# Performance work log

Hardware: AMD Instinct MI355X
Metric: run time of the kernel (lower is better)

The kernel has to match this reference:

```python
import jax, jax.numpy as jnp
import numpy as np

K = 3
KK = K * K


def _conv1x1(x, w, b):
    # x: [B,Ci,H,W], w: [Co,Ci]
    return jnp.einsum('bihw,oi->bohw', x, w) + b[None, :, None, None]


def _conv3x3(x, w, b):
    y = jax.lax.conv_general_dilated(x, w, (1, 1), ((1, 1), (1, 1)),
                                     dimension_numbers=('NCHW', 'OIHW', 'NCHW'))
    return y + b[None, :, None, None]


def _deform_conv3x3(x, offset, w, b):
    # Deformable conv v1, kernel 3x3, stride 1, pad 1, dilation 1, 1 deformable group.
    # x: [B,C,H,W]; offset: [B,2*KK,H,W] (dy,dx interleaved per kernel tap); w: [Co,C,3,3]
    B, C, H, W = x.shape
    dt = x.dtype
    off = offset.reshape(B, KK, 2, H, W)
    ky, kx = jnp.meshgrid(jnp.arange(K, dtype=dt), jnp.arange(K, dtype=dt), indexing='ij')
    ky = ky.reshape(KK)
    kx = kx.reshape(KK)
    # sampling locations: out_pos - pad + kernel_tap + learned offset
    base_y = jnp.arange(H, dtype=dt) - 1.0  # pad = 1
    base_x = jnp.arange(W, dtype=dt) - 1.0
    sy = base_y[None, None, :, None] + ky[None, :, None, None] + off[:, :, 0]  # [B,KK,H,W]
    sx = base_x[None, None, None, :] + kx[None, :, None, None] + off[:, :, 1]
    y0 = jnp.floor(sy)
    x0 = jnp.floor(sx)
    ty = sy - y0
    tx = sx - x0

    def gather(iy, ix):
        valid = ((iy >= 0) & (iy <= H - 1) & (ix >= 0) & (ix <= W - 1)).astype(dt)
        iyc = jnp.clip(iy, 0, H - 1).astype(jnp.int32)
        ixc = jnp.clip(ix, 0, W - 1).astype(jnp.int32)
        vals = jax.vmap(lambda img, a, c: img[:, a, c])(x, iyc, ixc)  # [B,C,KK,H,W]
        return vals * valid[:, None]

    w00 = ((1 - ty) * (1 - tx))[:, None]
    w01 = ((1 - ty) * tx)[:, None]
    w10 = (ty * (1 - tx))[:, None]
    w11 = (ty * tx)[:, None]
    sampled = (gather(y0, x0) * w00 + gather(y0, x0 + 1) * w01 +
               gather(y0 + 1, x0) * w10 + gather(y0 + 1, x0 + 1) * w11)  # [B,C,KK,H,W]
    Co = w.shape[0]
    out = jnp.einsum('bikhw,oik->bohw', sampled, w.reshape(Co, C, KK))
    return out + b[None, :, None, None]


def _branch(features, dw, db, ow, ob, tw, tb):
    h = _conv1x1(features, dw, db)
    off = _conv3x3(h, ow, ob)  # offset-predicting conv inside DFConv2d
    return jax.nn.relu(_deform_conv3x3(h, off, tw, tb))


def setup_inputs() -> dict:
    key = jax.random.key(0)
    ks = jax.random.split(key, 13)
    C = 256
    s1 = 1.0 / np.sqrt(C)          # kaiming_normal a=1 for 1x1 conv
    s3 = 1.0 / np.sqrt(C * KK)     # 3x3 conv
    so = 0.01                       # small offset-conv weights -> modest offsets
    f = lambda k, s, sc: jax.random.normal(k, s, dtype=jnp.float32) * sc
    return {
        'features': f(ks[0], (4, C, 64, 64), 1.0),
        'agg_down_w': f(ks[1], (C, C), s1),
        'agg_down_b': jnp.zeros((C,), jnp.float32),
        'agg_off_w': f(ks[2], (2 * KK, C, K, K), so),
        'agg_off_b': jnp.zeros((2 * KK,), jnp.float32),
        'agg_w': f(ks[3], (C, C, K, K), s3),
        'agg_b': jnp.zeros((C,), jnp.float32),
        'appr_down_w': f(ks[4], (C, C), s1),
        'appr_down_b': jnp.zeros((C,), jnp.float32),
        'appr_off_w': f(ks[5], (2 * KK, C, K, K), so),
        'appr_off_b': jnp.zeros((2 * KK,), jnp.float32),
        'appr_w': f(ks[6], (C, C, K, K), s3),
        'appr_b': jnp.zeros((C,), jnp.float32),
    }


def reference(features, agg_down_w, agg_down_b, agg_off_w, agg_off_b, agg_w, agg_b,
              appr_down_w, appr_down_b, appr_off_w, appr_off_b, appr_w, appr_b):
    agg = _branch(features, agg_down_w, agg_down_b, agg_off_w, agg_off_b, agg_w, agg_b)
    appr = _branch(features, appr_down_w, appr_down_b, appr_off_w, appr_off_b, appr_w, appr_b)
    return (agg, appr)
```

## Files before the change

### kernel.cpp

```cpp
#include <hip/hip_runtime.h>

#define HWP 4096
#define NPIX 4194304
#define KDIM 2304

typedef __attribute__((ext_vector_type(4))) float f32x4;
typedef __attribute__((ext_vector_type(4))) int   i32x4;
typedef __attribute__((ext_vector_type(8))) short short8;
typedef __attribute__((ext_vector_type(4))) unsigned short bf16x4;

__device__ __forceinline__ unsigned short bf16_rne(float f) {
    unsigned int u = __builtin_bit_cast(unsigned int, f);
    u += 0x7FFFu + ((u >> 16) & 1u);
    return (unsigned short)(u >> 16);
}

__device__ __forceinline__ float bf2f(unsigned short u) {
    return __builtin_bit_cast(float, (unsigned int)u << 16);
}

__device__ __forceinline__ unsigned int cvt_pk_bf16(float lo, float hi) {
    unsigned int r;
    asm("v_cvt_pk_bf16_f32 %0, %1, %2" : "=v"(r) : "v"(lo), "v"(hi));
    return r;
}

__device__ __forceinline__ void gload_lds16(const void* g, void* l) {
    __builtin_amdgcn_global_load_lds((const __attribute__((address_space(1))) void*)g,
                                     (__attribute__((address_space(3))) void*)l, 16, 0, 0);
}

__global__ void prep_all_kernel(const float* __restrict__ x, unsigned short* __restrict__ fbt,
                                const float* __restrict__ dw0, const float* __restrict__ dw1,
                                const float* __restrict__ tw0, const float* __restrict__ tw1,
                                const float* __restrict__ ow0, const float* __restrict__ ow1,
                                unsigned short* __restrict__ w1b2,
                                unsigned short* __restrict__ w2A,
                                unsigned short* __restrict__ w2o) {
    __shared__ float T[64][65];
    int b = blockIdx.x;
    int t = threadIdx.x;
    if (b < 1024) {
        int pt = b & 63, ct = (b >> 6) & 3, bb = b >> 8;
        int lane = t & 63;
        int r = t >> 6;
        int c0 = ct * 64, p0 = pt * 64;
        const float* xb = x + (size_t)(bb * 256 + c0) * HWP + p0;
#pragma unroll
        for (int rr = 0; rr < 16; ++rr) {
            int ci = r * 16 + rr;
            T[ci][lane] = xb[(size_t)ci * HWP + lane];
        }
        __syncthreads();
        unsigned short* ob = fbt + ((size_t)bb * HWP + p0) * 256 + c0;
#pragma unroll
        for (int rr = 0; rr < 16; ++rr) {
            int px = r * 16 + rr;
            ob[(size_t)px * 256 + lane] = bf16_rne(T[lane][px]);
        }
        return;
    }
    int idx = (b - 1024) * 256 + t;
    if (idx < 131072) {
        int br = idx >> 16;
        int i  = idx & 65535;
        const float* dw = br ? dw1 : dw0;
        w1b2[idx] = bf16_rne(dw[i]);
    } else if (idx < 131072 + 1179648) {
        int j = idx - 131072;
        int br = j >= 589824;
        int i  = br ? j - 589824 : j;
        const float* tw = br ? tw1 : tw0;
        int ci = i & 255;
        int r  = i >> 8;
        int tap = r % 9;
        int o   = r / 9;
        w2A[j] = bf16_rne(tw[(o * 256 + ci) * 9 + tap]);
    } else {
        int j = idx - 131072 - 1179648;
        int br = j >= 73728;
        int i  = br ? j - 73728 : j;
        const float* ow = br ? ow1 : ow0;
        int m = i / 2304;
        int k = i - m * 2304;
        int tap = k >> 8;
        int ci  = k & 255;
        w2o[j] = (m < 18) ? bf16_rne(ow[(m * 256 + ci) * 9 + tap]) : (unsigned short)0;
    }
}

__global__ void prep_w2_kernel(const float* __restrict__ tw0, const float* __restrict__ tw1,
                               unsigned short* __restrict__ w2) {
    int idx = blockIdx.x * 256 + threadIdx.x;
    int br = idx >= 589824;
    int i  = br ? idx - 589824 : idx;
    const float* tw = br ? tw1 : tw0;
    int ci = i & 255;
    int r  = i >> 8;
    int tap = r % 9;
    int o   = r / 9;
    w2[idx] = bf16_rne(tw[(o * 256 + ci) * 9 + tap]);
}

__global__ void prep_ow2_kernel(const float* __restrict__ ow0, const float* __restrict__ ow1,
                                float* __restrict__ owt) {
    int idx = blockIdx.x * 256 + threadIdx.x;
    int br = idx >= 41472;
    int i  = br ? idx - 41472 : idx;
    const float* ow = br ? ow1 : ow0;
    int co = i % 18;
    int r  = i / 18;
    int k  = r % 9;
    int ci = r / 9;
    owt[idx] = ow[(co * 256 + ci) * 9 + k];
}

__global__ void prep_w12_kernel(const float* __restrict__ dw0, const float* __restrict__ dw1,
                                unsigned short* __restrict__ w1b) {
    int idx = blockIdx.x * 256 + threadIdx.x;
    int br = idx >> 16;
    int i  = idx & 65535;
    const float* dw = br ? dw1 : dw0;
    w1b[idx] = bf16_rne(dw[i]);
}

__global__ void prep_fb16_kernel(const float* __restrict__ x, unsigned short* __restrict__ fbt) {
    __shared__ float T[64][65];
    int pt = blockIdx.x;
    int ct = blockIdx.y;
    int bb = blockIdx.z;
    int t = threadIdx.x;
    int lane = t & 63;
    int r = t >> 6;
    int c0 = ct * 64, p0 = pt * 64;
    const float* xb = x + (size_t)(bb * 256 + c0) * HWP + p0;
#pragma unroll
    for (int rr = 0; rr < 16; ++rr) {
        int ci = r * 16 + rr;
        T[ci][lane] = xb[(size_t)ci * HWP + lane];
    }
    __syncthreads();
    unsigned short* ob = fbt + ((size_t)bb * HWP + p0) * 256 + c0;
#pragma unroll
    for (int rr = 0; rr < 16; ++rr) {
        int px = r * 16 + rr;
        ob[(size_t)px * 256 + lane] = bf16_rne(T[lane][px]);
    }
}

__launch_bounds__(256)
__global__ void gemm1x1_kernel(const unsigned short* __restrict__ w1b2,
                               const unsigned short* __restrict__ fbt,
                               const float* __restrict__ db0, const float* __restrict__ db1,
                               float* __restrict__ h2, unsigned short* __restrict__ ht2,
                               int write_h) {
    __shared__ unsigned short As[128 * 64];
    __shared__ unsigned short Bs[64 * 64];
    int pt = blockIdx.x;
    int ot = blockIdx.y;
    int z  = blockIdx.z;
    int bb = z & 3;
    int br = z >> 2;
    const unsigned short* w1b = w1b2 + (size_t)br * 65536;
    const float* db = br ? db1 : db0;
    int t  = threadIdx.x;
    int l  = t & 63;
    int w  = t >> 6;
    int wr = w >> 1, wc = w & 1;
    int o0 = ot * 128, p0 = pt * 64;
    const unsigned short* fb = fbt + (size_t)bb * HWP * 256;
    f32x4 acc[4][2];
#pragma unroll
    for (int i = 0; i < 4; ++i)
#pragma unroll
        for (int j = 0; j < 2; ++j) acc[i][j] = (f32x4){0.f, 0.f, 0.f, 0.f};

    for (int ks = 0; ks < 4; ++ks) {
        int k0 = ks * 64;
#pragma unroll
        for (int rA = 0; rA < 4; ++rA) {
            int s = rA * 256 + t;
            int row = s >> 3, cg = (s & 7) ^ (row & 7);
            gload_lds16(w1b + (size_t)(o0 + row) * 256 + k0 + cg * 8, As + s * 8);
        }
#pragma unroll
        for (int rB = 0; rB < 2; ++rB) {
            int s = rB * 256 + t;
            int row = s >> 3, cg = (s & 7) ^ (row & 7);
            gload_lds16(fb + (size_t)(p0 + row) * 256 + k0 + cg * 8, Bs + s * 8);
        }
        __syncthreads();
#pragma unroll
        for (int half = 0; half < 2; ++half) {
            short8 a[4], b[2];
#pragma unroll
            for (int fr = 0; fr < 4; ++fr) {
                int row = wr * 64 + fr * 16 + (l & 15);
                int oct = half * 4 + (l >> 4);
                a[fr] = *reinterpret_cast<const short8*>(As + row * 64 + ((oct ^ (row & 7)) * 8));
            }
#pragma unroll
            for (int fc = 0; fc < 2; ++fc) {
                int row = wc * 32 + fc * 16 + (l & 15);
                int oct = half * 4 + (l >> 4);
                b[fc] = *reinterpret_cast<const short8*>(Bs + row * 64 + ((oct ^ (row & 7)) * 8));
            }
#pragma unroll
            for (int fr = 0; fr < 4; ++fr)
#pragma unroll
                for (int fc = 0; fc < 2; ++fc)
                    acc[fr][fc] = __builtin_amdgcn_mfma_f32_16x16x32_bf16(a[fr], b[fc], acc[fr][fc], 0, 0, 0);
        }
        __syncthreads();
    }

    float* hb = h2 + (size_t)br * NPIX + (size_t)bb * 256 * HWP;
    unsigned short* htb = ht2 + (size_t)br * NPIX + (size_t)bb * HWP * 256;
#pragma unroll
    for (int fr = 0; fr < 4; ++fr) {
        int o = o0 + wr * 64 + fr * 16 + ((l >> 4) << 2);
#pragma unroll
        for (int fc = 0; fc < 2; ++fc) {
            int p = p0 + wc * 32 + fc * 16 + (l & 15);
            f32x4 v;
#pragma unroll
            for (int reg = 0; reg < 4; ++reg) {
                v[reg] = acc[fr][fc][reg] + db[o + reg];
                if (write_h) hb[(size_t)(o + reg) * HWP + p] = v[reg];
            }
            uint2 pk;
            pk.x = cvt_pk_bf16(v[0], v[1]);
            pk.y = cvt_pk_bf16(v[2], v[3]);
            *reinterpret_cast<uint2*>(htb + (size_t)p * 256 + o) = pk;
        }
    }
}

__launch_bounds__(256)
__global__ void off_mfma_kernel(const unsigned short* __restrict__ w2o,
                                const unsigned short* __restrict__ ht2,
                                const float* __restrict__ ob0, const float* __restrict__ ob1,
                                float* __restrict__ off2) {
    __shared__ float red[4][1152];
    int id = blockIdx.x;
    int br = id >> 8;
    int bb = (id >> 6) & 3;
    int y  = id & 63;
    const unsigned short* wA = w2o + (size_t)br * 73728;
    const unsigned short* htb = ht2 + (size_t)br * NPIX + (size_t)bb * HWP * 256;
    const float* ob = br ? ob1 : ob0;
    int t = threadIdx.x;
    int l = t & 63;
    int w = t >> 6;
    short8 zero = {};
    f32x4 acc[2][4];
#pragma unroll
    for (int i = 0; i < 2; ++i)
#pragma unroll
        for (int j = 0; j < 4; ++j) acc[i][j] = (f32x4){0.f, 0.f, 0.f, 0.f};

    for (int tap = 0; tap < 9; ++tap) {
        int ky = tap / 3, kx = tap % 3;
        int yy = y + ky - 1;
        bool vy = (yy >= 0) && (yy < 64);
        int cyy = min(max(yy, 0), 63);
#pragma unroll
        for (int sh = 0; sh < 2; ++sh) {
            int s = w * 2 + sh;
            short8 a[2], b[4];
#pragma unroll
            for (int fr = 0; fr < 2; ++fr)
                a[fr] = *reinterpret_cast<const short8*>(
                    wA + (size_t)(fr * 16 + (l & 15)) * KDIM + tap * 256 + s * 32 + ((l >> 4) << 3));
#pragma unroll
            for (int fc = 0; fc < 4; ++fc) {
                int px = fc * 16 + (l & 15);
                int xx = px + kx - 1;
                bool v = vy && (xx >= 0) && (xx < 64);
                int cxx = min(max(xx, 0), 63);
                short8 bv = *reinterpret_cast<const short8*>(
                    htb + (size_t)(cyy * 64 + cxx) * 256 + s * 32 + ((l >> 4) << 3));
                b[fc] = v ? bv : zero;
            }
#pragma unroll
            for (int fr = 0; fr < 2; ++fr)
#pragma unroll
                for (int fc = 0; fc < 4; ++fc)
                    acc[fr][fc] = __builtin_amdgcn_mfma_f32_16x16x32_bf16(a[fr], b[fc], acc[fr][fc], 0, 0, 0);
        }
    }

#pragma unroll
    for (int fr = 0; fr < 2; ++fr)
#pragma unroll
        for (int fc = 0; fc < 4; ++fc) {
            int px = fc * 16 + (l & 15);
#pragma unroll
            for (int reg = 0; reg < 4; ++reg) {
                int co = fr * 16 + ((l >> 4) << 2) + reg;
                if (co < 18) red[w][co * 64 + px] = acc[fr][fc][reg];
            }
        }
    __syncthreads();
    float* offb = off2 + (size_t)br * 294912 + (size_t)(bb * 18) * HWP + y * 64;
    for (int e = t; e < 1152; e += 256) {
        int co = e >> 6, px = e & 63;
        float ssum = ob[co] + red[0][e] + red[1][e] + red[2][e] + red[3][e];
        offb[(size_t)co * HWP + px] = ssum;
    }
}

__global__ void off_conv_part_kernel(const float* __restrict__ h2, const float* __restrict__ owt2,
                                     float* __restrict__ part2) {
    int y  = blockIdx.x & 63;
    int bb = blockIdx.x >> 6;
    int c  = blockIdx.y;
    int br = blockIdx.z;
    const float* h = h2 + (size_t)br * NPIX;
    const float* owt = owt2 + (size_t)br * 41472;
    float* part = part2 + (size_t)br * 2359296;
    int t  = threadIdx.x;
    int x  = t & 63;
    int wv = __builtin_amdgcn_readfirstlane(t >> 6);
    int  toff[9];
    bool tval[9];
#pragma unroll
    for (int ky = 0; ky < 3; ++ky) {
        int yy = y + ky - 1;
        bool vy = (yy >= 0) && (yy < 64);
        int cyy = min(max(yy, 0), 63);
#pragma unroll
        for (int kx = 0; kx < 3; ++kx) {
            int xx = x + kx - 1;
            tval[ky * 3 + kx] = vy && (xx >= 0) && (xx < 64);
            toff[ky * 3 + kx] = cyy * 64 + min(max(xx, 0), 63);
        }
    }
    float acc[18];
#pragma unroll
    for (int co = 0; co < 18; ++co) acc[co] = 0.f;
    int ci0 = c * 32 + wv * 8;
    const float* hb = h + (size_t)(bb * 256 + ci0) * HWP;
#pragma unroll
    for (int i = 0; i < 8; ++i) {
        const float* hc = hb + i * HWP;
        const float* wci = owt + (size_t)(ci0 + i) * 162;
#pragma unroll
        for (int k = 0; k < 9; ++k) {
            float hv = hc[toff[k]];
            hv = tval[k] ? hv : 0.f;
            const float* wk = wci + k * 18;
#pragma unroll
            for (int co = 0; co < 18; ++co)
                acc[co] = fmaf(wk[co], hv, acc[co]);
        }
    }
    __shared__ float red[4][18][64];
    int wvl = t >> 6;
#pragma unroll
    for (int co = 0; co < 18; ++co) red[wvl][co][x] = acc[co];
    __syncthreads();
    if (wvl == 0) {
#pragma unroll
        for (int co = 0; co < 18; ++co) {
            float s = red[0][co][x] + red[1][co][x] + red[2][co][x] + red[3][co][x];
            part[(size_t)c * 294912 + ((bb * 18 + co) << 12) + (y << 6) + x] = s;
        }
    }
}

__global__ void off_reduce2_kernel(const float* __restrict__ part2,
                                   const float* __restrict__ ob0, const float* __restrict__ ob1,
                                   float* __restrict__ off2) {
    int idx = blockIdx.x * 256 + threadIdx.x;
    int br = idx >= 294912;
    int i  = br ? idx - 294912 : idx;
    const float* part = part2 + (size_t)br * 2359296;
    const float* b = br ? ob1 : ob0;
    int co = (i >> 12) % 18;
    float s = b[co];
#pragma unroll
    for (int c = 0; c < 8; ++c) s += part[(size_t)c * 294912 + i];
    off2[idx] = s;
}

__launch_bounds__(512, 4)
__global__ void dgemm_fused_kernel(const unsigned short* __restrict__ w2b,
                                   const unsigned short* __restrict__ ht2,
                                   const float* __restrict__ off2,
                                   const float* __restrict__ tb0,
                                   const float* __restrict__ tb1,
                                   float* __restrict__ out) {
    __shared__ unsigned short As[2][8][1024];
    __shared__ unsigned short Bs[64 * 256];
    int id = blockIdx.x;
    int sw = (id & 7) * 64 + (id >> 3);
    int br = sw >> 8;
    int mt = sw & 255;
    int bb = mt >> 6;
    int y  = mt & 63;
    const unsigned short* w2 = w2b + (size_t)br * 589824;
    const unsigned short* htb = ht2 + (size_t)br * NPIX + (size_t)bb * HWP * 256;
    const float* offb = off2 + (size_t)br * 294912 + (size_t)(bb * 18) * HWP + y * 64;
    const float* bias = br ? tb1 : tb0;
    int t = threadIdx.x;
    int l = t & 63;
    int w = t >> 6;
    int wvu = __builtin_amdgcn_readfirstlane(w);

    f32x4 acc[2][4];
#pragma unroll
    for (int i = 0; i < 2; ++i)
#pragma unroll
        for (int j = 0; j < 4; ++j) acc[i][j] = (f32x4){0.f, 0.f, 0.f, 0.f};

#define STAGE_AS(buf, ss)                                                          \
    do {                                                                           \
        _Pragma("unroll")                                                          \
        for (int r_ = 0; r_ < 2; ++r_) {                                           \
            int idx_ = r_ * 64 + l;                                                \
            int row_ = idx_ >> 2;                                                  \
            int kc_ = (idx_ & 3) ^ ((row_ >> 1) & 3);                              \
            gload_lds16(wtap + (size_t)(wvu * 32 + row_) * KDIM + (ss) * 32 + kc_ * 8, \
                        &As[buf][wvu][idx_ * 8]);                                  \
        }                                                                          \
    } while (0)

    for (int tap = 0; tap < 9; ++tap) {
        int ky = tap / 3, kx = tap % 3;
        const unsigned short* wtap = w2 + tap * 256;
        __syncthreads();
        STAGE_AS(0, 0);
#pragma unroll
        for (int i = 0; i < 8; ++i) {
            int px = wvu * 8 + i;
            float dy = offb[(size_t)(2 * tap) * HWP + px];
            float dx = offb[(size_t)(2 * tap + 1) * HWP + px];
            float sy = (float)(y - 1 + ky) + dy;
            float sx = (float)(px - 1 + kx) + dx;
            float y0f = floorf(sy), x0f = floorf(sx);
            float ty = sy - y0f, tx = sx - x0f;
            int iy0 = (int)y0f, ix0 = (int)x0f;
            int iy1 = iy0 + 1, ix1 = ix0 + 1;
            bool vy0 = (iy0 >= 0) & (iy0 < 64);
            bool vy1 = (iy1 >= 0) & (iy1 < 64);
            bool vx0 = (ix0 >= 0) & (ix0 < 64);
            bool vx1 = (ix1 >= 0) & (ix1 < 64);
            int cy0 = min(max(iy0, 0), 63), cy1 = min(max(iy1, 0), 63);
            int cx0 = min(max(ix0, 0), 63), cx1 = min(max(ix1, 0), 63);
            float w00 = (1.f - ty) * (1.f - tx) * ((vy0 & vx0) ? 1.f : 0.f);
            float w01 = (1.f - ty) * tx * ((vy0 & vx1) ? 1.f : 0.f);
            float w10 = ty * (1.f - tx) * ((vy1 & vx0) ? 1.f : 0.f);
            float w11 = ty * tx * ((vy1 & vx1) ? 1.f : 0.f);
            int le = l << 2;
            bf16x4 q00 = *reinterpret_cast<const bf16x4*>(htb + ((cy0 * 64 + cx0) << 8) + le);
            bf16x4 q01 = *reinterpret_cast<const bf16x4*>(htb + ((cy0 * 64 + cx1) << 8) + le);
            bf16x4 q10 = *reinterpret_cast<const bf16x4*>(htb + ((cy1 * 64 + cx0) << 8) + le);
            bf16x4 q11 = *reinterpret_cast<const bf16x4*>(htb + ((cy1 * 64 + cx1) << 8) + le);
            f32x4 s;
#pragma unroll
            for (int j = 0; j < 4; ++j)
                s[j] = fmaf(w00, bf2f(q00[j]),
                       fmaf(w01, bf2f(q01[j]),
                       fmaf(w10, bf2f(q10[j]), w11 * bf2f(q11[j]))));
            uint2 pk;
            pk.x = cvt_pk_bf16(s[0], s[1]);
            pk.y = cvt_pk_bf16(s[2], s[3]);
            int g = l >> 1, sub = l & 1;
            *reinterpret_cast<uint2*>(Bs + px * 256 + (((g ^ (px & 7)) << 3) | (sub << 2))) = pk;
        }
        __syncthreads();
        for (int s = 0; s < 8; ++s) {
            if (s < 7) {
                int buf = (s + 1) & 1;
                STAGE_AS(buf, s + 1);
            }
            asm volatile("s_waitcnt vmcnt(2)" ::: "memory");
            __builtin_amdgcn_sched_barrier(0);
            short8 a[2], b[4];
#pragma unroll
            for (int fr = 0; fr < 2; ++fr) {
                int rowl = fr * 16 + (l & 15);
                int oct = (l >> 4) ^ ((rowl >> 1) & 3);
                a[fr] = *reinterpret_cast<const short8*>(&As[s & 1][wvu][rowl * 32 + oct * 8]);
            }
#pragma unroll
            for (int fc = 0; fc < 4; ++fc) {
                int prow = fc * 16 + (l & 15);
                int cg8 = (s << 2) + (l >> 4);
                b[fc] = *reinterpret_cast<const short8*>(Bs + prow * 256 + ((cg8 ^ (prow & 7)) << 3));
            }
            __builtin_amdgcn_s_setprio(1);
#pragma unroll
            for (int fr = 0; fr < 2; ++fr)
#pragma unroll
                for (int fc = 0; fc < 4; ++fc)
                    acc[fr][fc] = __builtin_amdgcn_mfma_f32_16x16x32_bf16(a[fr], b[fc], acc[fr][fc], 0, 0, 0);
            __builtin_amdgcn_s_setprio(0);
        }
    }
#undef STAGE_AS

    float* outp = out + (size_t)br * NPIX + (size_t)(bb * 256) * HWP + y * 64;
#pragma unroll
    for (int fr = 0; fr < 2; ++fr) {
        int o = w * 32 + fr * 16 + ((l >> 4) << 2);
#pragma unroll
        for (int fc = 0; fc < 4; ++fc) {
            int pxc = fc * 16 + (l & 15);
#pragma unroll
            for (int reg = 0; reg < 4; ++reg) {
                float v = acc[fr][fc][reg] + bias[o + reg];
                outp[(size_t)(o + reg) * HWP + pxc] = fmaxf(v, 0.f);
            }
        }
    }
}

__launch_bounds__(256)
__global__ void sample2_kernel(const unsigned short* __restrict__ ht, const float* __restrict__ off,
                               unsigned short* __restrict__ sm, int b0) {
    int y   = blockIdx.x;
    int tap = blockIdx.y;
    int bb  = b0 + blockIdx.z;
    int t   = threadIdx.x;
    int lane = t & 63;
    int wv  = t >> 6;
    int ky = tap / 3, kx = tap % 3;
    const unsigned short* htb = ht + (size_t)bb * HWP * 256;
    const float* offy = off + ((bb * 18 + 2 * tap) * 64 + y) * 64;
    const float* offx = off + ((bb * 18 + 2 * tap + 1) * 64 + y) * 64;
    int mrow = ((bb - b0) * 64 + y) * 64;
#pragma unroll 4
    for (int i = 0; i < 16; ++i) {
        int px = wv * 16 + i;
        float dy = offy[px];
        float dx = offx[px];
        float sy = (float)(y - 1 + ky) + dy;
        float sx = (float)(px - 1 + kx) + dx;
        float y0f = floorf(sy), x0f = floorf(sx);
        float ty = sy - y0f, tx = sx - x0f;
        int iy0 = (int)y0f, ix0 = (int)x0f;
        int iy1 = iy0 + 1, ix1 = ix0 + 1;
        bool vy0 = (iy0 >= 0) & (iy0 < 64);
        bool vy1 = (iy1 >= 0) & (iy1 < 64);
        bool vx0 = (ix0 >= 0) & (ix0 < 64);
        bool vx1 = (ix1 >= 0) & (ix1 < 64);
        int cy0 = min(max(iy0, 0), 63), cy1 = min(max(iy1, 0), 63);
        int cx0 = min(max(ix0, 0), 63), cx1 = min(max(ix1, 0), 63);
        float w00 = (1.f - ty) * (1.f - tx) * ((vy0 & vx0) ? 1.f : 0.f);
        float w01 = (1.f - ty) * tx * ((vy0 & vx1) ? 1.f : 0.f);
        float w10 = ty * (1.f - tx) * ((vy1 & vx0) ? 1.f : 0.f);
        float w11 = ty * tx * ((vy1 & vx1) ? 1.f : 0.f);
        int le = lane << 2;
        bf16x4 q00 = *reinterpret_cast<const bf16x4*>(htb + ((cy0 * 64 + cx0) << 8) + le);
        bf16x4 q01 = *reinterpret_cast<const bf16x4*>(htb + ((cy0 * 64 + cx1) << 8) + le);
        bf16x4 q10 = *reinterpret_cast<const bf16x4*>(htb + ((cy1 * 64 + cx0) << 8) + le);
        bf16x4 q11 = *reinterpret_cast<const bf16x4*>(htb + ((cy1 * 64 + cx1) << 8) + le);
        f32x4 s;
#pragma unroll
        for (int j = 0; j < 4; ++j)
            s[j] = fmaf(w00, bf2f(q00[j]),
                   fmaf(w01, bf2f(q01[j]),
                   fmaf(w10, bf2f(q10[j]), w11 * bf2f(q11[j]))));
        uint2 pk;
        pk.x = cvt_pk_bf16(s[0], s[1]);
        pk.y = cvt_pk_bf16(s[2], s[3]);
        *reinterpret_cast<uint2*>(sm + (size_t)(mrow + px) * KDIM + tap * 256 + lane * 4) = pk;
    }
}

__launch_bounds__(256)
__global__ void gemm2_kernel(const unsigned short* __restrict__ w2b,
                             const unsigned short* __restrict__ smb, size_t smstride,
                             const float* __restrict__ tb0, const float* __restrict__ tb1,
                             float* __restrict__ out, int mbase) {
    __shared__ unsigned short As[128 * 64];
    __shared__ unsigned short Bs[64 * 64];
    int mt = blockIdx.x;
    int ot = blockIdx.y;
    int br = blockIdx.z;
    const unsigned short* w2 = w2b + (size_t)br * 589824;
    const unsigned short* sm = smb + (size_t)br * smstride;
    const float* bias = br ? tb1 : tb0;
    float* outp = out + (size_t)br * NPIX;
    int t  = threadIdx.x;
    int l  = t & 63;
    int w  = t >> 6;
    int wr = w >> 1, wc = w & 1;
    int o0 = ot * 128, m0 = mt * 64;
    f32x4 acc[4][2];
#pragma unroll
    for (int i = 0; i < 4; ++i)
#pragma unroll
        for (int j = 0; j < 2; ++j) acc[i][j] = (f32x4){0.f, 0.f, 0.f, 0.f};

    for (int ks = 0; ks < KDIM / 64; ++ks) {
        int k0 = ks * 64;
#pragma unroll
        for (int rA = 0; rA < 4; ++rA) {
            int s = rA * 256 + t;
            int row = s >> 3, cg = (s & 7) ^ (row & 7);
            gload_lds16(w2 + (size_t)(o0 + row) * KDIM + k0 + cg * 8, As + s * 8);
        }
#pragma unroll
        for (int rB = 0; rB < 2; ++rB) {
            int s = rB * 256 + t;
            int row = s >> 3, cg = (s & 7) ^ (row & 7);
            gload_lds16(sm + (size_t)(m0 + row) * KDIM + k0 + cg * 8, Bs + s * 8);
        }
        __syncthreads();
#pragma unroll
        for (int half = 0; half < 2; ++half) {
            short8 a[4], b[2];
#pragma unroll
            for (int fr = 0; fr < 4; ++fr) {
                int row = wr * 64 + fr * 16 + (l & 15);
                int oct = half * 4 + (l >> 4);
                a[fr] = *reinterpret_cast<const short8*>(As + row * 64 + ((oct ^ (row & 7)) * 8));
            }
#pragma unroll
            for (int fc = 0; fc < 2; ++fc) {
                int row = wc * 32 + fc * 16 + (l & 15);
                int oct = half * 4 + (l >> 4);
                b[fc] = *reinterpret_cast<const short8*>(Bs + row * 64 + ((oct ^ (row & 7)) * 8));
            }
#pragma unroll
            for (int fr = 0; fr < 4; ++fr)
#pragma unroll
                for (int fc = 0; fc < 2; ++fc)
                    acc[fr][fc] = __builtin_amdgcn_mfma_f32_16x16x32_bf16(a[fr], b[fc], acc[fr][fc], 0, 0, 0);
        }
        __syncthreads();
    }

#pragma unroll
    for (int fr = 0; fr < 4; ++fr) {
        int o = o0 + wr * 64 + fr * 16 + ((l >> 4) << 2);
#pragma unroll
        for (int fc = 0; fc < 2; ++fc) {
            int mg = mbase + m0 + wc * 32 + fc * 16 + (l & 15);
            int bbv = mg >> 12;
            int pix = mg & 4095;
            float* op = outp + (size_t)(bbv * 256) * HWP + pix;
#pragma unroll
            for (int reg = 0; reg < 4; ++reg) {
                float v = acc[fr][fc][reg] + bias[o + reg];
                op[(size_t)(o + reg) * HWP] = fmaxf(v, 0.f);
            }
        }
    }
}

extern "C" void kernel_launch(void* const* d_in, const int* in_sizes, int n_in,
                              void* d_out, int out_size, void* d_ws, size_t ws_size,
                              hipStream_t stream) {
    const float* feat = (const float*)d_in[0];
    char* base = (char*)d_ws;
    float* outp = (float*)d_out;
    const size_t perb = (size_t)HWP * KDIM * 2;

    const float* dw0 = (const float*)d_in[1];
    const float* db0 = (const float*)d_in[2];
    const float* ow0 = (const float*)d_in[3];
    const float* ob0 = (const float*)d_in[4];
    const float* tw0 = (const float*)d_in[5];
    const float* tb0 = (const float*)d_in[6];
    const float* dw1 = (const float*)d_in[7];
    const float* db1 = (const float*)d_in[8];
    const float* ow1 = (const float*)d_in[9];
    const float* ob1 = (const float*)d_in[10];
    const float* tw1 = (const float*)d_in[11];
    const float* tb1 = (const float*)d_in[12];

    bool tierA = ws_size >= 47218688;

    if (tierA) {
        unsigned short* ht2 = (unsigned short*)base;
        float* off2 = (float*)(base + 33554432);
        unsigned short* w2A = (unsigned short*)(base + 35913728);
        unsigned short* w2o = (unsigned short*)(base + 38273024);
        unsigned short* fbt = (unsigned short*)(base + 38567936);
        unsigned short* w1b2 = (unsigned short*)(base + 46956544);

        hipLaunchKernelGGL(prep_all_kernel, dim3(6720), dim3(256), 0, stream,
                           feat, fbt, dw0, dw1, tw0, tw1, ow0, ow1, w1b2, w2A, w2o);
        hipLaunchKernelGGL(gemm1x1_kernel, dim3(64, 2, 8), dim3(256), 0, stream,
                           w1b2, fbt, db0, db1, (float*)nullptr, ht2, 0);
        hipLaunchKernelGGL(off_mfma_kernel, dim3(512), dim3(256), 0, stream,
                           w2o, ht2, ob0, ob1, off2);
        hipLaunchKernelGGL(dgemm_fused_kernel, dim3(512), dim3(512), 0, stream,
                           w2A, ht2, off2, tb0, tb1, outp);
        return;
    }

    float* h   = (float*)base;
    float* off = h + NPIX;
    unsigned short* w2 = (unsigned short*)(base + 17956864);
    float* owt = (float*)(base + 19136512);
    unsigned short* ht = (unsigned short*)(base + 19302400);
    unsigned short* smN = (unsigned short*)(base + 27691008);
    float* partN = (float*)(base + 27691008);
    unsigned short* fbtN = (unsigned short*)(base + 27691008 + 9437184);
    unsigned short* w1bN = (unsigned short*)(base + 27691008 + 17825792);

    int nb = 0;
    if (27691008 + 4 * perb <= ws_size) nb = 4;
    else if (27691008 + 2 * perb <= ws_size) nb = 2;
    else nb = 1;

    for (int br = 0; br < 2; ++br) {
        const float* dw = (const float*)d_in[1 + 6 * br];
        const float* db = (const float*)d_in[2 + 6 * br];
        const float* ow = (const float*)d_in[3 + 6 * br];
        const float* ob = (const float*)d_in[4 + 6 * br];
        const float* tw = (const float*)d_in[5 + 6 * br];
        const float* tb = (const float*)d_in[6 + 6 * br];

        hipLaunchKernelGGL(prep_fb16_kernel, dim3(64, 4, 4), dim3(256), 0, stream, feat, fbtN);
        hipLaunchKernelGGL(prep_w12_kernel, dim3(256), dim3(256), 0, stream, dw, dw, w1bN);
        hipLaunchKernelGGL(gemm1x1_kernel, dim3(64, 2, 4), dim3(256), 0, stream,
                           w1bN, fbtN, db, db, h, ht, 1);
        hipLaunchKernelGGL(prep_ow2_kernel, dim3(162), dim3(256), 0, stream, ow, ow, owt);
        hipLaunchKernelGGL(off_conv_part_kernel, dim3(256, 8, 1), dim3(256), 0, stream,
                           h, owt, partN);
        hipLaunchKernelGGL(off_reduce2_kernel, dim3(1152), dim3(256), 0, stream,
                           partN, ob, ob, off);
        hipLaunchKernelGGL(prep_w2_kernel, dim3(2304), dim3(256), 0, stream, tw, tw, w2);

        for (int b0 = 0; b0 < 4; b0 += nb) {
            hipLaunchKernelGGL(sample2_kernel, dim3(64, 9, nb), dim3(256), 0, stream,
                               ht, off, smN, b0);
            hipLaunchKernelGGL(gemm2_kernel, dim3(nb * 64, 2, 1), dim3(256), 0, stream,
                               w2, smN, (size_t)0, tb, tb, outp + br * NPIX, b0 * HWP);
        }
    }
}
```

Baseline: 132.8 us.

## Precompute bilinear weights and corner indices in offset-conv epilogue

The offset-predicting kernel now turns its reduced offsets directly into per-tap, per-pixel bilinear weights (four floats, with out-of-bounds corners zeroed) and clamped corner pixel indices (four u16). It writes these into the workspace area that held the now-dead transposed features. The deformable GEMM kernel loads these values instead of recomputing floor, clamp, validity and weights for every tap, which shortens the VALU work between its gather loads. In exchange it adds about 7 MB of extra global writes and reads per call, and the uniform per-pixel loads may add latency to the gather phase.

```diff
diff --git a/kernel.cpp b/kernel.cpp
--- a/kernel.cpp
+++ b/kernel.cpp
@@ -8,6 +8,7 @@
 typedef __attribute__((ext_vector_type(4))) int   i32x4;
 typedef __attribute__((ext_vector_type(8))) short short8;
 typedef __attribute__((ext_vector_type(4))) unsigned short bf16x4;
+typedef __attribute__((ext_vector_type(4))) unsigned short u16x4;
 
 __device__ __forceinline__ unsigned short bf16_rne(float f) {
     unsigned int u = __builtin_bit_cast(unsigned int, f);
@@ -17,6 +18,14 @@
 
 __device__ __forceinline__ float bf2f(unsigned short u) {
     return __builtin_bit_cast(float, (unsigned int)u << 16);
+}
+
+__device__ __forceinline__ float u2f_lo(unsigned int u) {
+    return __builtin_bit_cast(float, u << 16);
+}
+
+__device__ __forceinline__ float u2f_hi(unsigned int u) {
+    return __builtin_bit_cast(float, u & 0xFFFF0000u);
 }
 
 __device__ __forceinline__ unsigned int cvt_pk_bf16(float lo, float hi) {
@@ -240,7 +249,7 @@
 __global__ void off_mfma_kernel(const unsigned short* __restrict__ w2o,
                                 const unsigned short* __restrict__ ht2,
                                 const float* __restrict__ ob0, const float* __restrict__ ob1,
-                                float* __restrict__ off2) {
+                                float* __restrict__ dwq, unsigned short* __restrict__ dcq) {
     __shared__ float red[4][1152];
     int id = blockIdx.x;
     int br = id >> 8;
@@ -302,11 +311,41 @@
             }
         }
     __syncthreads();
-    float* offb = off2 + (size_t)br * 294912 + (size_t)(bb * 18) * HWP + y * 64;
-    for (int e = t; e < 1152; e += 256) {
-        int co = e >> 6, px = e & 63;
-        float ssum = ob[co] + red[0][e] + red[1][e] + red[2][e] + red[3][e];
-        offb[(size_t)co * HWP + px] = ssum;
+
+    size_t dbase = ((size_t)(br * 4 + bb) * 9) * 4096 + (size_t)(y * 64);
+    for (int e = t; e < 576; e += 256) {
+        int tap = e >> 6, px = e & 63;
+        int c0 = 2 * tap, c1 = 2 * tap + 1;
+        float dy = ob[c0] + red[0][c0 * 64 + px] + red[1][c0 * 64 + px]
+                          + red[2][c0 * 64 + px] + red[3][c0 * 64 + px];
+        float dx = ob[c1] + red[0][c1 * 64 + px] + red[1][c1 * 64 + px]
+                          + red[2][c1 * 64 + px] + red[3][c1 * 64 + px];
+        int ky = tap / 3, kx = tap % 3;
+        float sy = (float)(y - 1 + ky) + dy;
+        float sx = (float)(px - 1 + kx) + dx;
+        float y0f = floorf(sy), x0f = floorf(sx);
+        float ty = sy - y0f, tx = sx - x0f;
+        int iy0 = (int)y0f, ix0 = (int)x0f;
+        int iy1 = iy0 + 1, ix1 = ix0 + 1;
+        bool vy0 = (iy0 >= 0) & (iy0 < 64);
+        bool vy1 = (iy1 >= 0) & (iy1 < 64);
+        bool vx0 = (ix0 >= 0) & (ix0 < 64);
+        bool vx1 = (ix1 >= 0) & (ix1 < 64);
+        int cy0 = min(max(iy0, 0), 63), cy1 = min(max(iy1, 0), 63);
+        int cx0 = min(max(ix0, 0), 63), cx1 = min(max(ix1, 0), 63);
+        f32x4 ww;
+        ww[0] = (1.f - ty) * (1.f - tx) * ((vy0 & vx0) ? 1.f : 0.f);
+        ww[1] = (1.f - ty) * tx * ((vy0 & vx1) ? 1.f : 0.f);
+        ww[2] = ty * (1.f - tx) * ((vy1 & vx0) ? 1.f : 0.f);
+        ww[3] = ty * tx * ((vy1 & vx1) ? 1.f : 0.f);
+        u16x4 pc;
+        pc[0] = (unsigned short)(cy0 * 64 + cx0);
+        pc[1] = (unsigned short)(cy0 * 64 + cx1);
+        pc[2] = (unsigned short)(cy1 * 64 + cx0);
+        pc[3] = (unsigned short)(cy1 * 64 + cx1);
+        size_t di = dbase + (size_t)tap * 4096 + px;
+        *reinterpret_cast<f32x4*>(dwq + di * 4) = ww;
+        *reinterpret_cast<u16x4*>(dcq + di * 4) = pc;
     }
 }
 
@@ -387,7 +426,8 @@
 __launch_bounds__(512, 4)
 __global__ void dgemm_fused_kernel(const unsigned short* __restrict__ w2b,
                                    const unsigned short* __restrict__ ht2,
-                                   const float* __restrict__ off2,
+                                   const float* __restrict__ dwq,
+                                   const unsigned short* __restrict__ dcq,
                                    const float* __restrict__ tb0,
                                    const float* __restrict__ tb1,
                                    float* __restrict__ out) {
@@ -401,12 +441,13 @@
     int y  = mt & 63;
     const unsigned short* w2 = w2b + (size_t)br * 589824;
     const unsigned short* htb = ht2 + (size_t)br * NPIX + (size_t)bb * HWP * 256;
-    const float* offb = off2 + (size_t)br * 294912 + (size_t)(bb * 18) * HWP + y * 64;
     const float* bias = br ? tb1 : tb0;
+    size_t dbase = ((size_t)(br * 4 + bb) * 9) * 4096 + (size_t)(y * 64);
     int t = threadIdx.x;
     int l = t & 63;
     int w = t >> 6;
     int wvu = __builtin_amdgcn_readfirstlane(w);
+    int le = l << 2;
 
     f32x4 acc[2][4];
 #pragma unroll
@@ -427,45 +468,39 @@
     } while (0)
 
     for (int tap = 0; tap < 9; ++tap) {
-        int ky = tap / 3, kx = tap % 3;
         const unsigned short* wtap = w2 + tap * 256;
+        const float* dwt = dwq + (dbase + (size_t)tap * 4096) * 4;
+        const unsigned short* dct = dcq + (dbase + (size_t)tap * 4096) * 4;
         __syncthreads();
         STAGE_AS(0, 0);
 #pragma unroll
         for (int i = 0; i < 8; ++i) {
             int px = wvu * 8 + i;
-            float dy = offb[(size_t)(2 * tap) * HWP + px];
-            float dx = offb[(size_t)(2 * tap + 1) * HWP + px];
-            float sy = (float)(y - 1 + ky) + dy;
-            float sx = (float)(px - 1 + kx) + dx;
-            float y0f = floorf(sy), x0f = floorf(sx);
-            float ty = sy - y0f, tx = sx - x0f;
-            int iy0 = (int)y0f, ix0 = (int)x0f;
-            int iy1 = iy0 + 1, ix1 = ix0 + 1;
-            bool vy0 = (iy0 >= 0) & (iy0 < 64);
-            bool vy1 = (iy1 >= 0) & (iy1 < 64);
-            bool vx0 = (ix0 >= 0) & (ix0 < 64);
-            bool vx1 = (ix1 >= 0) & (ix1 < 64);
-            int cy0 = min(max(iy0, 0), 63), cy1 = min(max(iy1, 0), 63);
-            int cx0 = min(max(ix0, 0), 63), cx1 = min(max(ix1, 0), 63);
-            float w00 = (1.f - ty) * (1.f - tx) * ((vy0 & vx0) ? 1.f : 0.f);
-            float w01 = (1.f - ty) * tx * ((vy0 & vx1) ? 1.f : 0.f);
-            float w10 = ty * (1.f - tx) * ((vy1 & vx0) ? 1.f : 0.f);
-            float w11 = ty * tx * ((vy1 & vx1) ? 1.f : 0.f);
-            int le = l << 2;
-            bf16x4 q00 = *reinterpret_cast<const bf16x4*>(htb + ((cy0 * 64 + cx0) << 8) + le);
-            bf16x4 q01 = *reinterpret_cast<const bf16x4*>(htb + ((cy0 * 64 + cx1) << 8) + le);
-            bf16x4 q10 = *reinterpret_cast<const bf16x4*>(htb + ((cy1 * 64 + cx0) << 8) + le);
-            bf16x4 q11 = *reinterpret_cast<const bf16x4*>(htb + ((cy1 * 64 + cx1) << 8) + le);
-            f32x4 s;
-#pragma unroll
-            for (int j = 0; j < 4; ++j)
-                s[j] = fmaf(w00, bf2f(q00[j]),
-                       fmaf(w01, bf2f(q01[j]),
-                       fmaf(w10, bf2f(q10[j]), w11 * bf2f(q11[j]))));
+            f32x4 ww = *reinterpret_cast<const f32x4*>(dwt + (size_t)px * 4);
+            u16x4 pc = *reinterpret_cast<const u16x4*>(dct + (size_t)px * 4);
+            int b00 = ((int)pc[0] << 8) + le;
+            int b01 = ((int)pc[1] << 8) + le;
+            int b10 = ((int)pc[2] << 8) + le;
+            int b11 = ((int)pc[3] << 8) + le;
+            uint2 u00 = *reinterpret_cast<const uint2*>(htb + b00);
+            uint2 u01 = *reinterpret_cast<const uint2*>(htb + b01);
+            uint2 u10 = *reinterpret_cast<const uint2*>(htb + b10);
+            uint2 u11 = *reinterpret_cast<const uint2*>(htb + b11);
+            float s0 = fmaf(ww[0], u2f_lo(u00.x),
+                       fmaf(ww[1], u2f_lo(u01.x),
+                       fmaf(ww[2], u2f_lo(u10.x), ww[3] * u2f_lo(u11.x))));
+            float s1 = fmaf(ww[0], u2f_hi(u00.x),
+                       fmaf(ww[1], u2f_hi(u01.x),
+                       fmaf(ww[2], u2f_hi(u10.x), ww[3] * u2f_hi(u11.x))));
+            float s2 = fmaf(ww[0], u2f_lo(u00.y),
+                       fmaf(ww[1], u2f_lo(u01.y),
+                       fmaf(ww[2], u2f_lo(u10.y), ww[3] * u2f_lo(u11.y))));
+            float s3 = fmaf(ww[0], u2f_hi(u00.y),
+                       fmaf(ww[1], u2f_hi(u01.y),
+                       fmaf(ww[2], u2f_hi(u10.y), ww[3] * u2f_hi(u11.y))));
             uint2 pk;
-            pk.x = cvt_pk_bf16(s[0], s[1]);
-            pk.y = cvt_pk_bf16(s[2], s[3]);
+            pk.x = cvt_pk_bf16(s0, s1);
+            pk.y = cvt_pk_bf16(s2, s3);
             int g = l >> 1, sub = l & 1;
             *reinterpret_cast<uint2*>(Bs + px * 256 + (((g ^ (px & 7)) << 3) | (sub << 2))) = pk;
         }
@@ -677,20 +712,21 @@
 
     if (tierA) {
         unsigned short* ht2 = (unsigned short*)base;
-        float* off2 = (float*)(base + 33554432);
         unsigned short* w2A = (unsigned short*)(base + 35913728);
         unsigned short* w2o = (unsigned short*)(base + 38273024);
         unsigned short* fbt = (unsigned short*)(base + 38567936);
         unsigned short* w1b2 = (unsigned short*)(base + 46956544);
+        float* dwq = (float*)(base + 38567936);
+        unsigned short* dcq = (unsigned short*)(base + 38567936 + 4718592);
 
         hipLaunchKernelGGL(prep_all_kernel, dim3(6720), dim3(256), 0, stream,
                            feat, fbt, dw0, dw1, tw0, tw1, ow0, ow1, w1b2, w2A, w2o);
         hipLaunchKernelGGL(gemm1x1_kernel, dim3(64, 2, 8), dim3(256), 0, stream,
                            w1b2, fbt, db0, db1, (float*)nullptr, ht2, 0);
         hipLaunchKernelGGL(off_mfma_kernel, dim3(512), dim3(256), 0, stream,
-                           w2o, ht2, ob0, ob1, off2);
+                           w2o, ht2, ob0, ob1, dwq, dcq);
         hipLaunchKernelGGL(dgemm_fused_kernel, dim3(512), dim3(512), 0, stream,
-                           w2A, ht2, off2, tb0, tb1, outp);
+                           w2A, ht2, dwq, dcq, tb0, tb1, outp);
         return;
     }
 
```

Result: faster. 127.0 us (-4.4%).
